# Kernel tuning notes

Measured on AMD Instinct MI355X. Metric: run time of the kernel, lower is better.

The kernel has to match this reference:

```python
import jax, jax.numpy as jnp
import numpy as np

N_NODES = 100000
N_EDGES = 1600000
IN_DIM, HID_DIM, OUT_DIM = 64, 128, 64


def setup_inputs() -> dict:
    key = jax.random.key(0)
    ks = jax.random.split(key, 12)
    s = 0.02
    x = jax.random.normal(ks[0], (N_NODES, IN_DIM), dtype=jnp.float32)
    edge_index = jax.random.randint(ks[1], (2, N_EDGES), 0, N_NODES, dtype=jnp.int64)
    return {
        "x": x,
        "edge_index": edge_index,
        # SAGEConv layer 1: lin_l (neighbors, with bias), lin_r (root, no bias)
        "w1l": jax.random.normal(ks[2], (HID_DIM, IN_DIM), dtype=jnp.float32) * s,
        "b1l": jnp.zeros((HID_DIM,), dtype=jnp.float32),
        "w1r": jax.random.normal(ks[3], (HID_DIM, IN_DIM), dtype=jnp.float32) * s,
        # SAGEConv layer 2
        "w2l": jax.random.normal(ks[4], (OUT_DIM, HID_DIM), dtype=jnp.float32) * s,
        "b2l": jnp.zeros((OUT_DIM,), dtype=jnp.float32),
        "w2r": jax.random.normal(ks[5], (OUT_DIM, HID_DIM), dtype=jnp.float32) * s,
        # classifier MLP: Linear(128,64) -> ReLU -> Linear(64,2) (dropout off in eval)
        "wc1": jax.random.normal(ks[6], (64, 2 * OUT_DIM), dtype=jnp.float32) * s,
        "bc1": jnp.zeros((64,), dtype=jnp.float32),
        "wc2": jax.random.normal(ks[7], (2, 64), dtype=jnp.float32) * s,
        "bc2": jnp.zeros((2,), dtype=jnp.float32),
    }


def _sage_conv(x, src, dst, wl, bl, wr):
    # PyG SAGEConv (aggr='mean'): out = lin_l(mean_{j in N(i)} x_j) + lin_r(x_i)
    msg = x[src]                                                  # [E, d] gather
    agg = jax.ops.segment_sum(msg, dst, num_segments=N_NODES)     # [N, d] scatter-add
    cnt = jax.ops.segment_sum(jnp.ones((src.shape[0],), x.dtype), dst, num_segments=N_NODES)
    mean = agg / jnp.maximum(cnt, 1.0)[:, None]
    return mean @ wl.T + bl + x @ wr.T


def reference(x, edge_index, w1l, b1l, w1r, w2l, b2l, w2r, wc1, bc1, wc2, bc2):
    src, dst = edge_index[0], edge_index[1]
    h = jax.nn.relu(_sage_conv(x, src, dst, w1l, b1l, w1r))   # dropout: eval mode (identity)
    h = jax.nn.relu(_sage_conv(h, src, dst, w2l, b2l, w2r))
    edge_repr = jnp.concatenate([h[src], h[dst]], axis=1)      # [E, 2*OUT_DIM]
    hidden = jax.nn.relu(edge_repr @ wc1.T + bc1)
    return hidden @ wc2.T + bc2                                 # [E, 2]
```

## Files before the change

kernel.cpp:

```cpp
#include <hip/hip_runtime.h>

#define N_NODES 100000
#define N_EDGES 1600000
#define NBLK_SCAN 391
#define SLICE_NODES 12500
#define BCAP 100000
#define EPB 2048
#define NBLK_BKT 782

typedef unsigned int uint;
typedef unsigned short ushort;
typedef __attribute__((ext_vector_type(8))) short bf16x8;
typedef __attribute__((ext_vector_type(4))) float f32x4;

__device__ inline float bflo(uint u) { union { uint i; float f; } c; c.i = u << 16; return c.f; }
__device__ inline float bfhi(uint u) { union { uint i; float f; } c; c.i = u & 0xffff0000u; return c.f; }
__device__ inline float bf2f(ushort h) { union { uint i; float f; } c; c.i = (uint)h << 16; return c.f; }
__device__ inline ushort f2bf(float f) {
    union { float f; uint u; } c; c.f = f;
    uint r = (c.u + 0x7fffu + ((c.u >> 16) & 1u)) >> 16;
    return (ushort)r;
}

#define W1_OFF   0
#define W2L_OFF  16384
#define W2R_OFF  24576
#define WC1_OFF  32768
#define W_TOTAL  40960

__global__ __launch_bounds__(256) void prep_weights(const float* __restrict__ w1r,
                                                    const float* __restrict__ w1l,
                                                    const float* __restrict__ w2l,
                                                    const float* __restrict__ w2r,
                                                    const float* __restrict__ wc1,
                                                    ushort* __restrict__ Whi,
                                                    ushort* __restrict__ Wlo) {
    int idx = blockIdx.x * 256 + threadIdx.x;
    if (idx >= W_TOTAL) return;
    float v;
    if (idx < W2L_OFF) {
        int o = idx >> 7, k = idx & 127;
        v = (k < 64) ? w1r[o * 64 + k] : w1l[o * 64 + (k - 64)];
    } else if (idx < W2R_OFF) {
        int t2 = idx - W2L_OFF; int o = t2 >> 7, k = t2 & 127;
        v = w2l[o * 128 + k];
    } else if (idx < WC1_OFF) {
        int t2 = idx - W2R_OFF; int o = t2 >> 7, k = t2 & 127;
        v = w2r[o * 128 + k];
    } else {
        int t2 = idx - WC1_OFF; int o = t2 >> 6, k = t2 & 63;
        v = wc1[(o & 63) * 128 + ((o >> 6) << 6) + k];
    }
    ushort hi = f2bf(v);
    ushort lo = f2bf(v - bf2f(hi));
    Whi[idx] = hi; Wlo[idx] = lo;
}

__global__ __launch_bounds__(256) void convert_kernel(const float* __restrict__ x,
                                                      ushort* __restrict__ xb) {
    int i = blockIdx.x * 256 + threadIdx.x;
    if (i < N_NODES * 32) {
        float2 v = ((const float2*)x)[i];
        uint o = (uint)f2bf(v.x) | ((uint)f2bf(v.y) << 16);
        ((uint*)xb)[i] = o;
    }
}

__global__ __launch_bounds__(256) void bucket_kernel(const int* __restrict__ src,
                                                     const int* __restrict__ dst,
                                                     int* __restrict__ cnt,
                                                     int* __restrict__ bcur,
                                                     uint* __restrict__ bkt) {
    __shared__ int hist[8], hist2[8], bbase[8];
    const int t = threadIdx.x;
    const int g = blockIdx.x & 7;
    const int ebase = blockIdx.x * EPB;
    const int eend = min(ebase + EPB, N_EDGES);
    if (t < 8) { hist[t] = 0; hist2[t] = 0; }
    __syncthreads();
    for (int e = ebase + t; e < eend; e += 256) {
        int d = dst[e];
        atomicAdd(&cnt[d], 1);
        atomicAdd(&hist[d / SLICE_NODES], 1);
    }
    __syncthreads();
    if (t < 8) bbase[t] = hist[t] ? atomicAdd(&bcur[g * 8 + t], hist[t]) : 0;
    __syncthreads();
    for (int e = ebase + t; e < eend; e += 256) {
        int d = dst[e], s = src[e];
        int b = d / SLICE_NODES;
        uint pack = ((uint)(d - b * SLICE_NODES) << 17) | (uint)s;
        int mo = atomicAdd(&hist2[b], 1);
        int pos = bbase[b] + mo;
        if (pos < BCAP) bkt[(size_t)(g * 8 + b) * BCAP + pos] = pack;
    }
}

__global__ __launch_bounds__(256) void scan_block_sums(const int* __restrict__ cnt,
                                                       int* __restrict__ partial) {
    __shared__ int red[4];
    int i = blockIdx.x * 256 + threadIdx.x;
    int v = (i < N_NODES) ? cnt[i] : 0;
#pragma unroll
    for (int off = 32; off; off >>= 1) v += __shfl_down(v, off, 64);
    if ((threadIdx.x & 63) == 0) red[threadIdx.x >> 6] = v;
    __syncthreads();
    if (threadIdx.x == 0) partial[blockIdx.x] = red[0] + red[1] + red[2] + red[3];
}

__global__ __launch_bounds__(512) void scan_top(int* __restrict__ partial) {
    __shared__ int s[512];
    int t = threadIdx.x;
    int orig = (t < NBLK_SCAN) ? partial[t] : 0;
    s[t] = orig;
    __syncthreads();
#pragma unroll
    for (int off = 1; off < 512; off <<= 1) {
        int v = (t >= off) ? s[t - off] : 0;
        __syncthreads();
        s[t] += v;
        __syncthreads();
    }
    if (t < NBLK_SCAN) partial[t] = s[t] - orig;
}

__global__ __launch_bounds__(256) void scan_final(const int* __restrict__ cnt,
                                                  const int* __restrict__ partial,
                                                  int* __restrict__ row_start,
                                                  int* __restrict__ cursor) {
    __shared__ int s[256];
    int i = blockIdx.x * 256 + threadIdx.x;
    int t = threadIdx.x;
    int orig = (i < N_NODES) ? cnt[i] : 0;
    s[t] = orig;
    __syncthreads();
#pragma unroll
    for (int off = 1; off < 256; off <<= 1) {
        int v = (t >= off) ? s[t - off] : 0;
        __syncthreads();
        s[t] += v;
        __syncthreads();
    }
    if (i < N_NODES) {
        int rs = partial[blockIdx.x] + s[t] - orig;
        row_start[i] = rs;
        cursor[i] = rs;
    }
}

__global__ __launch_bounds__(256) void fill_bucketed(const uint* __restrict__ bkt,
                                                     const int* __restrict__ bcur,
                                                     int* __restrict__ cursor,
                                                     int* __restrict__ nbr) {
    int s = blockIdx.x & 7;
    int g = (blockIdx.x >> 3) & 7;
    int chunk = blockIdx.x >> 6;
    int count = min(bcur[g * 8 + s], BCAP);
    int per = (count + 15) >> 4;
    int start = chunk * per;
    int end = min(start + per, count);
    const uint* B = bkt + (size_t)(g * 8 + s) * BCAP;
    for (int i = start + threadIdx.x; i < end; i += 256) {
        uint p = B[i];
        int d = s * SLICE_NODES + (int)(p >> 17);
        int pos = atomicAdd(&cursor[d], 1);
        nbr[pos] = (int)(p & 0x1FFFFu);
    }
}

__global__ __launch_bounds__(256) void agg_mean64_bf16(const int* __restrict__ row_start,
                                                       const int* __restrict__ cnt,
                                                       const int* __restrict__ nbr,
                                                       const ushort* __restrict__ feat,
                                                       float* __restrict__ outmean) {
    int node = blockIdx.x * 4 + (threadIdx.x >> 6);
    if (node >= N_NODES) return;
    int lane = threadIdx.x & 63;
    int half = lane >> 5;
    int f2   = lane & 31;
    int s = row_start[node];
    int d = cnt[node];
    float ax = 0.0f, ay = 0.0f;
    int p = 0;
    for (; p + 4 <= d; p += 4) {
        int n0 = nbr[s + p + half];
        int n1 = nbr[s + p + 2 + half];
        uint w0 = *(const uint*)(feat + (size_t)n0 * 64 + f2 * 2);
        uint w1 = *(const uint*)(feat + (size_t)n1 * 64 + f2 * 2);
        ax += bflo(w0) + bflo(w1);
        ay += bfhi(w0) + bfhi(w1);
    }
    for (; p + 2 <= d; p += 2) {
        int n0 = nbr[s + p + half];
        uint w0 = *(const uint*)(feat + (size_t)n0 * 64 + f2 * 2);
        ax += bflo(w0);
        ay += bfhi(w0);
    }
    if (p < d && half == 0) {
        int n0 = nbr[s + p];
        uint w0 = *(const uint*)(feat + (size_t)n0 * 64 + f2 * 2);
        ax += bflo(w0);
        ay += bfhi(w0);
    }
    ax += __shfl_xor(ax, 32, 64);
    ay += __shfl_xor(ay, 32, 64);
    if (half == 0) {
        float inv = 1.0f / fmaxf((float)d, 1.0f);
        float2 o; o.x = ax * inv; o.y = ay * inv;
        *(float2*)&outmean[(size_t)node * 64 + f2 * 2] = o;
    }
}

#define MFMA __builtin_amdgcn_mfma_f32_16x16x32_bf16

__global__ __launch_bounds__(256) void g1g2_kernel(const float* __restrict__ x,
                                                   const float* __restrict__ mean1,
                                                   const ushort* __restrict__ Whi,
                                                   const ushort* __restrict__ Wlo,
                                                   const float* __restrict__ b1l,
                                                   ushort* __restrict__ h1hi,
                                                   ushort* __restrict__ y2b) {
    __shared__ ushort Ah[64 * 136];
    __shared__ ushort Al[64 * 136];
    const int t = threadIdx.x;
    const int l = t & 63;
    const int wv = t >> 6;
    const int base = blockIdx.x * 64;
    const int lr = l & 15;
    const int lk = (l >> 4) * 8;

    for (int idx = t; idx < 2048; idx += 256) {
        int halfsel = idx >> 10;
        int id2 = idx & 1023;
        int n = id2 >> 4;
        int k0 = (id2 & 15) * 4;
        int gn = base + n;
        float4 v = make_float4(0.f, 0.f, 0.f, 0.f);
        if (gn < N_NODES) v = *(const float4*)&(halfsel ? mean1 : x)[(size_t)gn * 64 + k0];
        ushort h0 = f2bf(v.x), h1_ = f2bf(v.y), h2_ = f2bf(v.z), h3 = f2bf(v.w);
        ushort l0 = f2bf(v.x - bf2f(h0)), l1 = f2bf(v.y - bf2f(h1_));
        ushort l2 = f2bf(v.z - bf2f(h2_)), l3 = f2bf(v.w - bf2f(h3));
        int col = halfsel * 64 + k0;
        uint2 ph; ph.x = (uint)h0 | ((uint)h1_ << 16); ph.y = (uint)h2_ | ((uint)h3 << 16);
        uint2 pl; pl.x = (uint)l0 | ((uint)l1 << 16); pl.y = (uint)l2 | ((uint)l3 << 16);
        *(uint2*)&Ah[n * 136 + col] = ph;
        *(uint2*)&Al[n * 136 + col] = pl;
    }
    __syncthreads();

    f32x4 acc[4][2];
#pragma unroll
    for (int m4 = 0; m4 < 4; ++m4)
#pragma unroll
        for (int n2 = 0; n2 < 2; ++n2) acc[m4][n2] = (f32x4){0.f, 0.f, 0.f, 0.f};

#pragma unroll
    for (int ks = 0; ks < 4; ++ks) {
        bf16x8 ah[4], al[4];
        int aoff = lr * 136 + ks * 32 + lk;
#pragma unroll
        for (int m4 = 0; m4 < 4; ++m4) {
            ah[m4] = *(const bf16x8*)&Ah[m4 * 2176 + aoff];
            al[m4] = *(const bf16x8*)&Al[m4 * 2176 + aoff];
        }
#pragma unroll
        for (int n2 = 0; n2 < 2; ++n2) {
            int o = wv * 32 + n2 * 16 + lr;
            int woff = W1_OFF + o * 128 + ks * 32 + lk;
            bf16x8 bh = *(const bf16x8*)&Whi[woff];
            bf16x8 bl = *(const bf16x8*)&Wlo[woff];
#pragma unroll
            for (int m4 = 0; m4 < 4; ++m4) {
                acc[m4][n2] = MFMA(al[m4], bh, acc[m4][n2], 0, 0, 0);
                acc[m4][n2] = MFMA(ah[m4], bl, acc[m4][n2], 0, 0, 0);
                acc[m4][n2] = MFMA(ah[m4], bh, acc[m4][n2], 0, 0, 0);
            }
        }
    }
    __syncthreads();
    ushort* H1h = Ah;
    ushort* H1l = Al;

#pragma unroll
    for (int n2 = 0; n2 < 2; ++n2) {
        int o = wv * 32 + n2 * 16 + lr;
        float bb = b1l[o];
#pragma unroll
        for (int m4 = 0; m4 < 4; ++m4) {
#pragma unroll
            for (int r = 0; r < 4; ++r) {
                int nl = m4 * 16 + (l >> 4) * 4 + r;
                float val = fmaxf(acc[m4][n2][r] + bb, 0.f);
                ushort hi = f2bf(val);
                ushort lo = f2bf(val - bf2f(hi));
                H1h[nl * 136 + o] = hi;
                H1l[nl * 136 + o] = lo;
            }
        }
    }
    __syncthreads();

    for (int idx = t; idx < 2048; idx += 256) {
        int n = idx >> 5;
        int c4 = (idx & 31) * 4;
        int gn = base + n;
        if (gn < N_NODES)
            *(uint2*)&h1hi[(size_t)gn * 128 + c4] = *(uint2*)&H1h[n * 136 + c4];
    }

    f32x4 acc2[4];
#pragma unroll
    for (int m4 = 0; m4 < 4; ++m4) acc2[m4] = (f32x4){0.f, 0.f, 0.f, 0.f};
#pragma unroll
    for (int ks = 0; ks < 4; ++ks) {
        int aoff = lr * 136 + ks * 32 + lk;
        int o2 = wv * 16 + lr;
        int woff = W2L_OFF + o2 * 128 + ks * 32 + lk;
        bf16x8 bh = *(const bf16x8*)&Whi[woff];
        bf16x8 bl = *(const bf16x8*)&Wlo[woff];
#pragma unroll
        for (int m4 = 0; m4 < 4; ++m4) {
            bf16x8 ah = *(const bf16x8*)&H1h[m4 * 2176 + aoff];
            bf16x8 al = *(const bf16x8*)&H1l[m4 * 2176 + aoff];
            acc2[m4] = MFMA(al, bh, acc2[m4], 0, 0, 0);
            acc2[m4] = MFMA(ah, bl, acc2[m4], 0, 0, 0);
            acc2[m4] = MFMA(ah, bh, acc2[m4], 0, 0, 0);
        }
    }
#pragma unroll
    for (int m4 = 0; m4 < 4; ++m4) {
#pragma unroll
        for (int r = 0; r < 4; ++r) {
            int nl = m4 * 16 + (l >> 4) * 4 + r;
            int gn = base + nl;
            if (gn < N_NODES) y2b[(size_t)gn * 64 + wv * 16 + lr] = f2bf(acc2[m4][r]);
        }
    }
}

__global__ __launch_bounds__(256) void g3g4_kernel(const ushort* __restrict__ h1hi,
                                                   const float* __restrict__ mean2,
                                                   const ushort* __restrict__ Whi,
                                                   const ushort* __restrict__ Wlo,
                                                   const float* __restrict__ b2l,
                                                   const float* __restrict__ bc1,
                                                   ushort* __restrict__ uvb) {
    __shared__ ushort H1h[64 * 136];
    __shared__ float  M2[64 * 68];
    __shared__ ushort H2l[64 * 72];
    const int t = threadIdx.x;
    const int l = t & 63;
    const int wv = t >> 6;
    const int base = blockIdx.x * 64;
    const int lr = l & 15;
    const int lk = (l >> 4) * 8;

    for (int idx = t; idx < 2048; idx += 256) {
        int n = idx >> 5;
        int c4 = (idx & 31) * 4;
        int gn = base + n;
        uint2 vh = make_uint2(0u, 0u);
        if (gn < N_NODES) vh = *(const uint2*)&h1hi[(size_t)gn * 128 + c4];
        *(uint2*)&H1h[n * 136 + c4] = vh;
    }
    for (int idx = t; idx < 1024; idx += 256) {
        int n = idx >> 4;
        int k0 = (idx & 15) * 4;
        int gn = base + n;
        float4 v = make_float4(0.f, 0.f, 0.f, 0.f);
        if (gn < N_NODES) v = *(const float4*)&mean2[(size_t)gn * 64 + k0];
        *(float4*)&M2[n * 68 + k0] = v;
    }
    __syncthreads();

    f32x4 acc[4];
#pragma unroll
    for (int m4 = 0; m4 < 4; ++m4) acc[m4] = (f32x4){0.f, 0.f, 0.f, 0.f};
#pragma unroll
    for (int ks = 0; ks < 4; ++ks) {
        int aoff = lr * 136 + ks * 32 + lk;
        int o2 = wv * 16 + lr;
        int woff = W2R_OFF + o2 * 128 + ks * 32 + lk;
        bf16x8 bh = *(const bf16x8*)&Whi[woff];
        bf16x8 bl = *(const bf16x8*)&Wlo[woff];
#pragma unroll
        for (int m4 = 0; m4 < 4; ++m4) {
            bf16x8 ah = *(const bf16x8*)&H1h[m4 * 2176 + aoff];
            acc[m4] = MFMA(ah, bl, acc[m4], 0, 0, 0);
            acc[m4] = MFMA(ah, bh, acc[m4], 0, 0, 0);
        }
    }
    __syncthreads();
    ushort* H2h = H1h;

    {
        int o2 = wv * 16 + lr;
        float bb = b2l[o2];
#pragma unroll
        for (int m4 = 0; m4 < 4; ++m4) {
#pragma unroll
            for (int r = 0; r < 4; ++r) {
                int nl = m4 * 16 + (l >> 4) * 4 + r;
                float val = fmaxf(acc[m4][r] + M2[nl * 68 + o2] + bb, 0.f);
                ushort hi = f2bf(val);
                ushort lo = f2bf(val - bf2f(hi));
                H2h[nl * 72 + o2] = hi;
                H2l[nl * 72 + o2] = lo;
            }
        }
    }
    __syncthreads();

    f32x4 acc4[4][2];
#pragma unroll
    for (int m4 = 0; m4 < 4; ++m4)
#pragma unroll
        for (int n2 = 0; n2 < 2; ++n2) acc4[m4][n2] = (f32x4){0.f, 0.f, 0.f, 0.f};
#pragma unroll
    for (int ks = 0; ks < 2; ++ks) {
        bf16x8 ah[4], al[4];
        int aoff = lr * 72 + ks * 32 + lk;
#pragma unroll
        for (int m4 = 0; m4 < 4; ++m4) {
            ah[m4] = *(const bf16x8*)&H2h[m4 * 1152 + aoff];
            al[m4] = *(const bf16x8*)&H2l[m4 * 1152 + aoff];
        }
#pragma unroll
        for (int n2 = 0; n2 < 2; ++n2) {
            int o = wv * 32 + n2 * 16 + lr;
            int woff = WC1_OFF + o * 64 + ks * 32 + lk;
            bf16x8 bh = *(const bf16x8*)&Whi[woff];
            bf16x8 bl = *(const bf16x8*)&Wlo[woff];
#pragma unroll
            for (int m4 = 0; m4 < 4; ++m4) {
                acc4[m4][n2] = MFMA(al[m4], bh, acc4[m4][n2], 0, 0, 0);
                acc4[m4][n2] = MFMA(ah[m4], bl, acc4[m4][n2], 0, 0, 0);
                acc4[m4][n2] = MFMA(ah[m4], bh, acc4[m4][n2], 0, 0, 0);
            }
        }
    }
#pragma unroll
    for (int n2 = 0; n2 < 2; ++n2) {
        int o = wv * 32 + n2 * 16 + lr;
        float bb = (o < 64) ? bc1[o] : 0.0f;
#pragma unroll
        for (int m4 = 0; m4 < 4; ++m4) {
#pragma unroll
            for (int r = 0; r < 4; ++r) {
                int nl = m4 * 16 + (l >> 4) * 4 + r;
                int gn = base + nl;
                if (gn < N_NODES) uvb[(size_t)gn * 128 + o] = f2bf(acc4[m4][n2][r] + bb);
            }
        }
    }
}

__global__ __launch_bounds__(256) void edge_kernel(const int* __restrict__ src,
                                                   const int* __restrict__ dst,
                                                   const ushort* __restrict__ uvb,
                                                   const float* __restrict__ wc2,
                                                   const float* __restrict__ bc2,
                                                   float* __restrict__ out) {
    int e = blockIdx.x * blockDim.x + threadIdx.x;
    if (e >= N_EDGES) return;
    const uint4* ua = (const uint4*)(uvb + (size_t)src[e] * 128);
    const uint4* va = (const uint4*)(uvb + (size_t)dst[e] * 128 + 64);
    float o0 = 0.0f, o1 = 0.0f;
#pragma unroll
    for (int k = 0; k < 8; ++k) {
        uint4 a = ua[k], b = va[k];
        int i0 = k * 8;
        float h0, h1v;
        h0 = fmaxf(bflo(a.x) + bflo(b.x), 0.f); h1v = fmaxf(bfhi(a.x) + bfhi(b.x), 0.f);
        o0 += wc2[i0] * h0 + wc2[i0 + 1] * h1v;  o1 += wc2[64 + i0] * h0 + wc2[65 + i0] * h1v;
        h0 = fmaxf(bflo(a.y) + bflo(b.y), 0.f); h1v = fmaxf(bfhi(a.y) + bfhi(b.y), 0.f);
        o0 += wc2[i0 + 2] * h0 + wc2[i0 + 3] * h1v;  o1 += wc2[66 + i0] * h0 + wc2[67 + i0] * h1v;
        h0 = fmaxf(bflo(a.z) + bflo(b.z), 0.f); h1v = fmaxf(bfhi(a.z) + bfhi(b.z), 0.f);
        o0 += wc2[i0 + 4] * h0 + wc2[i0 + 5] * h1v;  o1 += wc2[68 + i0] * h0 + wc2[69 + i0] * h1v;
        h0 = fmaxf(bflo(a.w) + bflo(b.w), 0.f); h1v = fmaxf(bfhi(a.w) + bfhi(b.w), 0.f);
        o0 += wc2[i0 + 6] * h0 + wc2[i0 + 7] * h1v;  o1 += wc2[70 + i0] * h0 + wc2[71 + i0] * h1v;
    }
    float2 r;
    r.x = o0 + bc2[0];
    r.y = o1 + bc2[1];
    *(float2*)(out + (size_t)e * 2) = r;
}

extern "C" void kernel_launch(void* const* d_in, const int* in_sizes, int n_in,
                              void* d_out, int out_size, void* d_ws, size_t ws_size,
                              hipStream_t stream) {
    const float* x   = (const float*)d_in[0];
    const int*   ei  = (const int*)d_in[1];
    const float* w1l = (const float*)d_in[2];
    const float* b1l = (const float*)d_in[3];
    const float* w1r = (const float*)d_in[4];
    const float* w2l = (const float*)d_in[5];
    const float* b2l = (const float*)d_in[6];
    const float* w2r = (const float*)d_in[7];
    const float* wc1 = (const float*)d_in[8];
    const float* bc1 = (const float*)d_in[9];
    const float* wc2 = (const float*)d_in[10];
    const float* bc2 = (const float*)d_in[11];
    float* out = (float*)d_out;

    const int* srcp = ei;
    const int* dstp = ei + N_EDGES;

    float*  ws    = (float*)d_ws;
    ushort* xb    = (ushort*)ws;
    ushort* y2b   = (ushort*)ws;
    float*  mean1 = ws + 3200000;
    ushort* uvb   = (ushort*)(ws + 3200000);
    ushort* h1hi  = (ushort*)(ws + 9600000);
    uint*   bkt   = (uint*)(ws + 16000000);
    float*  mean2 = ws + 22400000;
    int*    ib    = (int*)(ws + 28800000);
    int* cnt       = ib;
    int* row_start = ib + 100000;
    int* cursor    = ib + 200000;
    int* partial   = ib + 300000;
    int* bcur      = ib + 300512;
    int* nbr       = ib + 300576;
    ushort* Whi = (ushort*)(ws + 30800000);
    ushort* Wlo = (ushort*)(ws + 30900000);

    hipMemsetAsync(cnt, 0, (size_t)N_NODES * 4, stream);
    hipMemsetAsync(bcur, 0, 64 * 4, stream);

    prep_weights<<<(W_TOTAL + 255) / 256, 256, 0, stream>>>(w1r, w1l, w2l, w2r, wc1, Whi, Wlo);
    convert_kernel<<<12500, 256, 0, stream>>>(x, xb);

    bucket_kernel<<<NBLK_BKT, 256, 0, stream>>>(srcp, dstp, cnt, bcur, bkt);
    scan_block_sums<<<NBLK_SCAN, 256, 0, stream>>>(cnt, partial);
    scan_top<<<1, 512, 0, stream>>>(partial);
    scan_final<<<NBLK_SCAN, 256, 0, stream>>>(cnt, partial, row_start, cursor);
    fill_bucketed<<<1024, 256, 0, stream>>>(bkt, bcur, cursor, nbr);

    const int NAB = (N_NODES + 3) / 4;
    const int NB  = (N_NODES + 63) / 64;

    agg_mean64_bf16<<<NAB, 256, 0, stream>>>(row_start, cnt, nbr, xb, mean1);
    g1g2_kernel<<<NB, 256, 0, stream>>>(x, mean1, Whi, Wlo, b1l, h1hi, y2b);
    agg_mean64_bf16<<<NAB, 256, 0, stream>>>(row_start, cnt, nbr, y2b, mean2);
    g3g4_kernel<<<NB, 256, 0, stream>>>(h1hi, mean2, Whi, Wlo, b2l, bc1, uvb);
    edge_kernel<<<(N_EDGES + 255) / 256, 256, 0, stream>>>(srcp, dstp, uvb, wc2, bc2, out);
}
```

Baseline: 448.5 us.

## Split node features into quarter-column tables for cache-local neighbor aggregation

```diff
diff --git a/kernel.cpp b/kernel.cpp
--- a/kernel.cpp
+++ b/kernel.cpp
@@ -7,11 +7,13 @@
 #define BCAP 100000
 #define EPB 2048
 #define NBLK_BKT 782
+#define AGG_BPP 3125
 
 typedef unsigned int uint;
 typedef unsigned short ushort;
 typedef __attribute__((ext_vector_type(8))) short bf16x8;
 typedef __attribute__((ext_vector_type(4))) float f32x4;
+typedef __attribute__((ext_vector_type(2))) float f32x2;
 
 __device__ inline float bflo(uint u) { union { uint i; float f; } c; c.i = u << 16; return c.f; }
 __device__ inline float bfhi(uint u) { union { uint i; float f; } c; c.i = u & 0xffff0000u; return c.f; }
@@ -56,19 +58,19 @@
     Whi[idx] = hi; Wlo[idx] = lo;
 }
 
-__global__ __launch_bounds__(256) void convert_kernel(const float* __restrict__ x,
-                                                      ushort* __restrict__ xb) {
+__global__ __launch_bounds__(256) void convert_q(const float* __restrict__ x,
+                                                 ushort* __restrict__ xq) {
     int i = blockIdx.x * 256 + threadIdx.x;
-    if (i < N_NODES * 32) {
-        float2 v = ((const float2*)x)[i];
-        uint o = (uint)f2bf(v.x) | ((uint)f2bf(v.y) << 16);
-        ((uint*)xb)[i] = o;
-    }
+    if (i >= N_NODES * 32) return;
+    int n = i >> 5, dw = i & 31;
+    int q = dw >> 3, j = dw & 7;
+    float2 v = *(const float2*)&x[(size_t)n * 64 + dw * 2];
+    uint o = (uint)f2bf(v.x) | ((uint)f2bf(v.y) << 16);
+    ((uint*)xq)[((size_t)q * N_NODES + n) * 8 + j] = o;
 }
 
 __global__ __launch_bounds__(256) void bucket_kernel(const int* __restrict__ src,
                                                      const int* __restrict__ dst,
-                                                     int* __restrict__ cnt,
                                                      int* __restrict__ bcur,
                                                      uint* __restrict__ bkt) {
     __shared__ int hist[8], hist2[8], bbase[8];
@@ -79,9 +81,7 @@
     if (t < 8) { hist[t] = 0; hist2[t] = 0; }
     __syncthreads();
     for (int e = ebase + t; e < eend; e += 256) {
-        int d = dst[e];
-        atomicAdd(&cnt[d], 1);
-        atomicAdd(&hist[d / SLICE_NODES], 1);
+        atomicAdd(&hist[dst[e] / SLICE_NODES], 1);
     }
     __syncthreads();
     if (t < 8) bbase[t] = hist[t] ? atomicAdd(&bcur[g * 8 + t], hist[t]) : 0;
@@ -93,6 +93,24 @@
         int mo = atomicAdd(&hist2[b], 1);
         int pos = bbase[b] + mo;
         if (pos < BCAP) bkt[(size_t)(g * 8 + b) * BCAP + pos] = pack;
+    }
+}
+
+__global__ __launch_bounds__(256) void cnt_sliced(const uint* __restrict__ bkt,
+                                                  const int* __restrict__ bcur,
+                                                  int* __restrict__ cnt) {
+    int s = blockIdx.x & 7;
+    int g = (blockIdx.x >> 3) & 7;
+    int chunk = blockIdx.x >> 6;
+    int count = min(bcur[g * 8 + s], BCAP);
+    int per = (count + 15) >> 4;
+    int start = chunk * per;
+    int end = min(start + per, count);
+    const uint* B = bkt + (size_t)(g * 8 + s) * BCAP;
+    int base = s * SLICE_NODES;
+    for (int i = start + threadIdx.x; i < end; i += 256) {
+        uint p = __builtin_nontemporal_load(&B[i]);
+        atomicAdd(&cnt[base + (int)(p >> 17)], 1);
     }
 }
 
@@ -161,65 +179,58 @@
     int end = min(start + per, count);
     const uint* B = bkt + (size_t)(g * 8 + s) * BCAP;
     for (int i = start + threadIdx.x; i < end; i += 256) {
-        uint p = B[i];
+        uint p = __builtin_nontemporal_load(&B[i]);
         int d = s * SLICE_NODES + (int)(p >> 17);
         int pos = atomicAdd(&cursor[d], 1);
         nbr[pos] = (int)(p & 0x1FFFFu);
     }
 }
 
-__global__ __launch_bounds__(256) void agg_mean64_bf16(const int* __restrict__ row_start,
-                                                       const int* __restrict__ cnt,
-                                                       const int* __restrict__ nbr,
-                                                       const ushort* __restrict__ feat,
-                                                       float* __restrict__ outmean) {
-    int node = blockIdx.x * 4 + (threadIdx.x >> 6);
-    if (node >= N_NODES) return;
-    int lane = threadIdx.x & 63;
-    int half = lane >> 5;
-    int f2   = lane & 31;
-    int s = row_start[node];
-    int d = cnt[node];
-    float ax = 0.0f, ay = 0.0f;
-    int p = 0;
-    for (; p + 4 <= d; p += 4) {
-        int n0 = nbr[s + p + half];
-        int n1 = nbr[s + p + 2 + half];
-        uint w0 = *(const uint*)(feat + (size_t)n0 * 64 + f2 * 2);
-        uint w1 = *(const uint*)(feat + (size_t)n1 * 64 + f2 * 2);
-        ax += bflo(w0) + bflo(w1);
-        ay += bfhi(w0) + bfhi(w1);
-    }
-    for (; p + 2 <= d; p += 2) {
-        int n0 = nbr[s + p + half];
-        uint w0 = *(const uint*)(feat + (size_t)n0 * 64 + f2 * 2);
-        ax += bflo(w0);
-        ay += bfhi(w0);
-    }
-    if (p < d && half == 0) {
-        int n0 = nbr[s + p];
-        uint w0 = *(const uint*)(feat + (size_t)n0 * 64 + f2 * 2);
-        ax += bflo(w0);
-        ay += bfhi(w0);
-    }
-    ax += __shfl_xor(ax, 32, 64);
-    ay += __shfl_xor(ay, 32, 64);
-    if (half == 0) {
-        float inv = 1.0f / fmaxf((float)d, 1.0f);
-        float2 o; o.x = ax * inv; o.y = ay * inv;
-        *(float2*)&outmean[(size_t)node * 64 + f2 * 2] = o;
+__global__ __launch_bounds__(256) void agg_mean_q(const int* __restrict__ row_start,
+                                                  const int* __restrict__ cnt,
+                                                  const int* __restrict__ nbr,
+                                                  const ushort* __restrict__ featq,
+                                                  ushort* __restrict__ meanq) {
+    int q = blockIdx.x / AGG_BPP;
+    int b = blockIdx.x % AGG_BPP;
+    const uint* tab = (const uint*)featq + (size_t)q * N_NODES * 8;
+    uint* outp = (uint*)meanq + (size_t)q * N_NODES * 8;
+    int l = threadIdx.x & 63;
+    int wv = threadIdx.x >> 6;
+    int g8 = l >> 3, j = l & 7;
+    int node0 = b * 32 + wv * 8;
+#pragma unroll 1
+    for (int nn = 0; nn < 8; ++nn) {
+        int node = node0 + nn;
+        int s = row_start[node];
+        int d = cnt[node];
+        float ax = 0.f, ay = 0.f;
+#pragma unroll 1
+        for (int p = g8; p < d; p += 8) {
+            int nb = __builtin_nontemporal_load(&nbr[s + p]);
+            uint w = tab[(size_t)nb * 8 + j];
+            ax += bflo(w); ay += bfhi(w);
+        }
+        ax += __shfl_xor(ax, 8, 64);  ay += __shfl_xor(ay, 8, 64);
+        ax += __shfl_xor(ax, 16, 64); ay += __shfl_xor(ay, 16, 64);
+        ax += __shfl_xor(ax, 32, 64); ay += __shfl_xor(ay, 32, 64);
+        if (g8 == 0) {
+            float inv = 1.0f / fmaxf((float)d, 1.0f);
+            uint o = (uint)f2bf(ax * inv) | ((uint)f2bf(ay * inv) << 16);
+            __builtin_nontemporal_store(o, &outp[(size_t)node * 8 + j]);
+        }
     }
 }
 
 #define MFMA __builtin_amdgcn_mfma_f32_16x16x32_bf16
 
 __global__ __launch_bounds__(256) void g1g2_kernel(const float* __restrict__ x,
-                                                   const float* __restrict__ mean1,
+                                                   const ushort* __restrict__ mean1q,
                                                    const ushort* __restrict__ Whi,
                                                    const ushort* __restrict__ Wlo,
                                                    const float* __restrict__ b1l,
                                                    ushort* __restrict__ h1hi,
-                                                   ushort* __restrict__ y2b) {
+                                                   ushort* __restrict__ y2q) {
     __shared__ ushort Ah[64 * 136];
     __shared__ ushort Al[64 * 136];
     const int t = threadIdx.x;
@@ -229,22 +240,29 @@
     const int lr = l & 15;
     const int lk = (l >> 4) * 8;
 
-    for (int idx = t; idx < 2048; idx += 256) {
-        int halfsel = idx >> 10;
-        int id2 = idx & 1023;
-        int n = id2 >> 4;
-        int k0 = (id2 & 15) * 4;
+    for (int idx = t; idx < 1024; idx += 256) {
+        int n = idx >> 4;
+        int k0 = (idx & 15) * 4;
         int gn = base + n;
         float4 v = make_float4(0.f, 0.f, 0.f, 0.f);
-        if (gn < N_NODES) v = *(const float4*)&(halfsel ? mean1 : x)[(size_t)gn * 64 + k0];
+        if (gn < N_NODES) v = *(const float4*)&x[(size_t)gn * 64 + k0];
         ushort h0 = f2bf(v.x), h1_ = f2bf(v.y), h2_ = f2bf(v.z), h3 = f2bf(v.w);
         ushort l0 = f2bf(v.x - bf2f(h0)), l1 = f2bf(v.y - bf2f(h1_));
         ushort l2 = f2bf(v.z - bf2f(h2_)), l3 = f2bf(v.w - bf2f(h3));
-        int col = halfsel * 64 + k0;
         uint2 ph; ph.x = (uint)h0 | ((uint)h1_ << 16); ph.y = (uint)h2_ | ((uint)h3 << 16);
         uint2 pl; pl.x = (uint)l0 | ((uint)l1 << 16); pl.y = (uint)l2 | ((uint)l3 << 16);
-        *(uint2*)&Ah[n * 136 + col] = ph;
-        *(uint2*)&Al[n * 136 + col] = pl;
+        *(uint2*)&Ah[n * 136 + k0] = ph;
+        *(uint2*)&Al[n * 136 + k0] = pl;
+    }
+    for (int idx = t; idx < 1024; idx += 256) {
+        int n = idx >> 4;
+        int c4 = (idx & 15) * 4;
+        int gn = base + n;
+        int q = c4 >> 4, off = c4 & 15;
+        uint2 vh = make_uint2(0u, 0u);
+        if (gn < N_NODES) vh = *(const uint2*)&mean1q[((size_t)q * N_NODES + gn) * 16 + off];
+        *(uint2*)&Ah[n * 136 + 64 + c4] = vh;
+        *(uint2*)&Al[n * 136 + 64 + c4] = make_uint2(0u, 0u);
     }
     __syncthreads();
 
@@ -333,13 +351,14 @@
         for (int r = 0; r < 4; ++r) {
             int nl = m4 * 16 + (l >> 4) * 4 + r;
             int gn = base + nl;
-            if (gn < N_NODES) y2b[(size_t)gn * 64 + wv * 16 + lr] = f2bf(acc2[m4][r]);
+            if (gn < N_NODES)
+                y2q[((size_t)wv * N_NODES + gn) * 16 + lr] = f2bf(acc2[m4][r]);
         }
     }
 }
 
 __global__ __launch_bounds__(256) void g3g4_kernel(const ushort* __restrict__ h1hi,
-                                                   const float* __restrict__ mean2,
+                                                   const ushort* __restrict__ mean2q,
                                                    const ushort* __restrict__ Whi,
                                                    const ushort* __restrict__ Wlo,
                                                    const float* __restrict__ b2l,
@@ -365,11 +384,14 @@
     }
     for (int idx = t; idx < 1024; idx += 256) {
         int n = idx >> 4;
-        int k0 = (idx & 15) * 4;
+        int c4 = (idx & 15) * 4;
         int gn = base + n;
-        float4 v = make_float4(0.f, 0.f, 0.f, 0.f);
-        if (gn < N_NODES) v = *(const float4*)&mean2[(size_t)gn * 64 + k0];
-        *(float4*)&M2[n * 68 + k0] = v;
+        int q = c4 >> 4, off = c4 & 15;
+        uint2 vh = make_uint2(0u, 0u);
+        if (gn < N_NODES) vh = *(const uint2*)&mean2q[((size_t)q * N_NODES + gn) * 16 + off];
+        float4 mv;
+        mv.x = bflo(vh.x); mv.y = bfhi(vh.x); mv.z = bflo(vh.y); mv.w = bfhi(vh.y);
+        *(float4*)&M2[n * 68 + c4] = mv;
     }
     __syncthreads();
 
@@ -463,8 +485,10 @@
                                                    float* __restrict__ out) {
     int e = blockIdx.x * blockDim.x + threadIdx.x;
     if (e >= N_EDGES) return;
-    const uint4* ua = (const uint4*)(uvb + (size_t)src[e] * 128);
-    const uint4* va = (const uint4*)(uvb + (size_t)dst[e] * 128 + 64);
+    int se = __builtin_nontemporal_load(&src[e]);
+    int de = __builtin_nontemporal_load(&dst[e]);
+    const uint4* ua = (const uint4*)(uvb + (size_t)se * 128);
+    const uint4* va = (const uint4*)(uvb + (size_t)de * 128 + 64);
     float o0 = 0.0f, o1 = 0.0f;
 #pragma unroll
     for (int k = 0; k < 8; ++k) {
@@ -480,10 +504,10 @@
         h0 = fmaxf(bflo(a.w) + bflo(b.w), 0.f); h1v = fmaxf(bfhi(a.w) + bfhi(b.w), 0.f);
         o0 += wc2[i0 + 6] * h0 + wc2[i0 + 7] * h1v;  o1 += wc2[70 + i0] * h0 + wc2[71 + i0] * h1v;
     }
-    float2 r;
+    f32x2 r;
     r.x = o0 + bc2[0];
     r.y = o1 + bc2[1];
-    *(float2*)(out + (size_t)e * 2) = r;
+    __builtin_nontemporal_store(r, (f32x2*)(out + (size_t)e * 2));
 }
 
 extern "C" void kernel_launch(void* const* d_in, const int* in_sizes, int n_in,
@@ -506,15 +530,15 @@
     const int* srcp = ei;
     const int* dstp = ei + N_EDGES;
 
-    float*  ws    = (float*)d_ws;
-    ushort* xb    = (ushort*)ws;
-    ushort* y2b   = (ushort*)ws;
-    float*  mean1 = ws + 3200000;
-    ushort* uvb   = (ushort*)(ws + 3200000);
-    ushort* h1hi  = (ushort*)(ws + 9600000);
-    uint*   bkt   = (uint*)(ws + 16000000);
-    float*  mean2 = ws + 22400000;
-    int*    ib    = (int*)(ws + 28800000);
+    float*  ws     = (float*)d_ws;
+    ushort* xq     = (ushort*)ws;
+    ushort* y2q    = (ushort*)ws;
+    ushort* mean1q = (ushort*)(ws + 3200000);
+    ushort* uvb    = (ushort*)(ws + 3200000);
+    ushort* h1hi   = (ushort*)(ws + 9600000);
+    uint*   bkt    = (uint*)(ws + 16000000);
+    ushort* mean2q = (ushort*)(ws + 22400000);
+    int*    ib     = (int*)(ws + 28800000);
     int* cnt       = ib;
     int* row_start = ib + 100000;
     int* cursor    = ib + 200000;
@@ -528,20 +552,20 @@
     hipMemsetAsync(bcur, 0, 64 * 4, stream);
 
     prep_weights<<<(W_TOTAL + 255) / 256, 256, 0, stream>>>(w1r, w1l, w2l, w2r, wc1, Whi, Wlo);
-    convert_kernel<<<12500, 256, 0, stream>>>(x, xb);
-
-    bucket_kernel<<<NBLK_BKT, 256, 0, stream>>>(srcp, dstp, cnt, bcur, bkt);
+    convert_q<<<12500, 256, 0, stream>>>(x, xq);
+
+    bucket_kernel<<<NBLK_BKT, 256, 0, stream>>>(srcp, dstp, bcur, bkt);
+    cnt_sliced<<<1024, 256, 0, stream>>>(bkt, bcur, cnt);
     scan_block_sums<<<NBLK_SCAN, 256, 0, stream>>>(cnt, partial);
     scan_top<<<1, 512, 0, stream>>>(partial);
     scan_final<<<NBLK_SCAN, 256, 0, stream>>>(cnt, partial, row_start, cursor);
     fill_bucketed<<<1024, 256, 0, stream>>>(bkt, bcur, cursor, nbr);
 
-    const int NAB = (N_NODES + 3) / 4;
-    const int NB  = (N_NODES + 63) / 64;
-
-    agg_mean64_bf16<<<NAB, 256, 0, stream>>>(row_start, cnt, nbr, xb, mean1);
-    g1g2_kernel<<<NB, 256, 0, stream>>>(x, mean1, Whi, Wlo, b1l, h1hi, y2b);
-    agg_mean64_bf16<<<NAB, 256, 0, stream>>>(row_start, cnt, nbr, y2b, mean2);
-    g3g4_kernel<<<NB, 256, 0, stream>>>(h1hi, mean2, Whi, Wlo, b2l, bc1, uvb);
+    const int NB = (N_NODES + 63) / 64;
+
+    agg_mean_q<<<4 * AGG_BPP, 256, 0, stream>>>(row_start, cnt, nbr, xq, mean1q);
+    g1g2_kernel<<<NB, 256, 0, stream>>>(x, mean1q, Whi, Wlo, b1l, h1hi, y2q);
+    agg_mean_q<<<4 * AGG_BPP, 256, 0, stream>>>(row_start, cnt, nbr, y2q, mean2q);
+    g3g4_kernel<<<NB, 256, 0, stream>>>(h1hi, mean2q, Whi, Wlo, b2l, bc1, uvb);
     edge_kernel<<<(N_EDGES + 255) / 256, 256, 0, stream>>>(srcp, dstp, uvb, wc2, bc2, out);
 }
```

After: 650.0 us. 1.45x slower.
